# Optimization experiments

Measured on AMD Instinct MI355X. Metric: run time of the kernel, lower is better.

## Reference

```python
import jax, jax.numpy as jnp
import numpy as np

E = 512      # embed_size
H = 8        # num_heads
L = 4        # num_layers
SF = 4       # sparsity_factor
F_IN = 128   # input feature dim (nn.Linear(128, embed_size))
N_CLS = 10


def setup_inputs() -> dict:
    key = jax.random.key(0)
    ks = jax.random.split(key, 14)
    B, S = 8, 1024
    s = 0.02
    inp = {
        "x": jax.random.normal(ks[0], (B, S, F_IN), jnp.float32),
        "emb_w": jax.random.normal(ks[1], (F_IN, E), jnp.float32) * s,
        "emb_b": jnp.zeros((E,), jnp.float32),
        "Wq": jax.random.normal(ks[2], (L, E, E), jnp.float32) * s,
        "Wk": jax.random.normal(ks[3], (L, E, E), jnp.float32) * s,
        "Wv": jax.random.normal(ks[4], (L, E, E), jnp.float32) * s,
        "Wo": jax.random.normal(ks[5], (L, E, E), jnp.float32) * s,
        "bq": jnp.zeros((L, E), jnp.float32),
        "bk": jnp.zeros((L, E), jnp.float32),
        "bv": jnp.zeros((L, E), jnp.float32),
        "bo": jnp.zeros((L, E), jnp.float32),
        "fc_w": jax.random.normal(ks[6], (E, N_CLS), jnp.float32) * s,
        "fc_b": jnp.zeros((N_CLS,), jnp.float32),
    }
    return inp


def _sparse_attn(h, wq, wk, wv, wo, bq, bk, bv, bo):
    # One SparseAttention layer: per-query top-k sparsified multi-head attention.
    B, S, _ = h.shape
    d = E // H
    k = max(1, S // SF)  # keep top S/sparsity_factor keys per query
    scale = 1.0 / np.sqrt(d)

    def heads(t):  # [B,S,E] -> [B,H,S,d]
        return t.reshape(B, S, H, d).transpose(0, 2, 1, 3)

    q = heads(h @ wq + bq)
    kk = heads(h @ wk + bk)
    v = heads(h @ wv + bv)

    scores = jnp.einsum('bhqd,bhkd->bhqk', q, kk) * scale  # [B,H,S,S]
    thresh = jax.lax.top_k(scores, k)[0][..., -1:]          # k-th largest per query
    scores = jnp.where(scores >= thresh, scores, jnp.float32(-1e9))
    p = jax.nn.softmax(scores, axis=-1)
    o = jnp.einsum('bhqk,bhkd->bhqd', p, v)                 # [B,H,S,d]
    o = o.transpose(0, 2, 1, 3).reshape(B, S, E)
    return o @ wo + bo


def reference(x, emb_w, emb_b, Wq, Wk, Wv, Wo, bq, bk, bv, bo, fc_w, fc_b):
    h = x @ emb_w + emb_b  # [B,S,E]
    for l in range(L):
        h = _sparse_attn(h, Wq[l], Wk[l], Wv[l], Wo[l], bq[l], bk[l], bv[l], bo[l])
    return h.mean(axis=1) @ fc_w + fc_b  # [B,10]
```

## Files before the change

kernel.cpp:

```cpp
#include <hip/hip_runtime.h>

#define EDIM 512
#define NH 8
#define HD 64
#define SEQ 1024
#define BATCH 8
#define NLAYER 4
#define KSEL 256
#define PQ 8

typedef __attribute__((ext_vector_type(8))) short short8;
typedef __attribute__((ext_vector_type(4))) float f32x4;

__device__ __forceinline__ unsigned short bf16_rne(float f) {
    unsigned u = __float_as_uint(f);
    return (unsigned short)((u + 0x7FFFu + ((u >> 16) & 1u)) >> 16);
}
__device__ __forceinline__ float bf16_tof(unsigned short h) {
    return __uint_as_float(((unsigned)h) << 16);
}
__device__ __forceinline__ void split2(float f, unsigned short& hi, unsigned short& lo) {
    hi = bf16_rne(f);
    float r = f - bf16_tof(hi);
    lo = (unsigned short)(__float_as_uint(r) >> 16);
}
__device__ __forceinline__ void split8(const float* xs, short8& hi, short8& lo) {
#pragma unroll
    for (int j = 0; j < 8; ++j) {
        unsigned short h, lw;
        split2(xs[j], h, lw);
        hi[j] = (short)h; lo[j] = (short)lw;
    }
}
__device__ __forceinline__ unsigned fmap(float s) {
    int fi = __float_as_int(s);
    return (unsigned)(fi ^ ((fi >> 31) | 0x80000000));
}
__device__ __forceinline__ float funmap(unsigned u) {
    int fi = (u & 0x80000000u) ? (int)(u ^ 0x80000000u) : (int)~u;
    return __int_as_float(fi);
}

__global__ __launch_bounds__(256) void conv_a(const float* __restrict__ A,
                                              short* __restrict__ af, int K)
{
    const int t = threadIdx.x, l = t & 63;
    const int KC = K >> 5;
    const int kc = blockIdx.x * 4 + (t >> 6);
    const int mt = blockIdx.y;
    const int m = mt * 16 + (l & 15);
    const int kb = kc * 32 + ((l >> 4) << 3);
    float4 x0 = *(const float4*)(A + (size_t)m * K + kb);
    float4 x1 = *(const float4*)(A + (size_t)m * K + kb + 4);
    float xs[8] = {x0.x, x0.y, x0.z, x0.w, x1.x, x1.y, x1.z, x1.w};
    short8 hi, lo;
    split8(xs, hi, lo);
    short* dst = af + (size_t)((mt * KC + kc) * 2) * 512 + l * 8;
    *(short8*)(dst) = hi;
    *(short8*)(dst + 512) = lo;
}

__global__ __launch_bounds__(256) void conv_wall(const float* __restrict__ Wq,
                                                 const float* __restrict__ Wk,
                                                 const float* __restrict__ Wv,
                                                 const float* __restrict__ Wo,
                                                 short* __restrict__ wf)
{
    const int z = blockIdx.z;
    const int layer = z >> 2, mm = z & 3;
    const float* W = (mm == 0 ? Wq : mm == 1 ? Wk : mm == 2 ? Wv : Wo)
                     + (size_t)layer * EDIM * EDIM;
    const int t = threadIdx.x, l = t & 63;
    const int kc = blockIdx.x * 4 + (t >> 6);
    const int nt = blockIdx.y;
    const int n = nt * 16 + (l & 15);
    const int kb = kc * 32 + ((l >> 4) << 3);
    float xs[8];
#pragma unroll
    for (int j = 0; j < 8; ++j) xs[j] = W[(size_t)(kb + j) * EDIM + n];
    short8 hi, lo;
    split8(xs, hi, lo);
    short* dst = wf + (size_t)z * 524288 + (size_t)((nt * 16 + kc) * 2) * 512 + l * 8;
    *(short8*)(dst) = hi;
    *(short8*)(dst + 512) = lo;
}

__global__ __launch_bounds__(256) void conv_w1(const float* __restrict__ W,
                                               short* __restrict__ wf, int K, int N)
{
    const int t = threadIdx.x, l = t & 63;
    const int KC = K >> 5;
    const int kc = blockIdx.x * 4 + (t >> 6);
    const int nt = blockIdx.y;
    const int n = nt * 16 + (l & 15);
    const int kb = kc * 32 + ((l >> 4) << 3);
    float xs[8];
#pragma unroll
    for (int j = 0; j < 8; ++j) xs[j] = W[(size_t)(kb + j) * N + n];
    short8 hi, lo;
    split8(xs, hi, lo);
    short* dst = wf + (size_t)((nt * KC + kc) * 2) * 512 + l * 8;
    *(short8*)(dst) = hi;
    *(short8*)(dst + 512) = lo;
}

__global__ __launch_bounds__(256, 3) void gemm_af(const short* __restrict__ af_in,
                                                  const short* __restrict__ wf,
                                                  const float* __restrict__ bias,
                                                  float* __restrict__ Cout,
                                                  short* __restrict__ af_out,
                                                  int K)
{
    __shared__ float S[128 * 68];
    const int t = threadIdx.x, l = t & 63, w = t >> 6;
    const int KC = K >> 5;
    const int mt0 = blockIdx.x * 8 + (w & 1) * 4;
    const int nt0l = (w >> 1) * 2;
    f32x4 acc[4][2] = {};

#pragma unroll 2
    for (int kc = 0; kc < KC; ++kc) {
        short8 ah[4], al[4], bh[2], bl[2];
#pragma unroll
        for (int i = 0; i < 4; ++i) {
            const short* ap = af_in + (size_t)(((mt0 + i) * KC + kc) * 2) * 512 + l * 8;
            ah[i] = *(const short8*)(ap);
            al[i] = *(const short8*)(ap + 512);
        }
#pragma unroll
        for (int j = 0; j < 2; ++j) {
            const short* bp = wf + (size_t)(((blockIdx.y * 4 + nt0l + j) * KC + kc) * 2) * 512 + l * 8;
            bh[j] = *(const short8*)(bp);
            bl[j] = *(const short8*)(bp + 512);
        }
#pragma unroll
        for (int i = 0; i < 4; ++i)
#pragma unroll
            for (int j = 0; j < 2; ++j) {
                acc[i][j] = __builtin_amdgcn_mfma_f32_16x16x32_bf16(ah[i], bh[j], acc[i][j], 0, 0, 0);
                acc[i][j] = __builtin_amdgcn_mfma_f32_16x16x32_bf16(ah[i], bl[j], acc[i][j], 0, 0, 0);
                acc[i][j] = __builtin_amdgcn_mfma_f32_16x16x32_bf16(al[i], bh[j], acc[i][j], 0, 0, 0);
            }
    }
#pragma unroll
    for (int j = 0; j < 2; ++j) {
        const int cl = (nt0l + j) * 16 + (l & 15);
        const float bv = bias[blockIdx.y * 64 + cl];
#pragma unroll
        for (int i = 0; i < 4; ++i) {
            const int rl = ((w & 1) * 4 + i) * 16 + ((l >> 4) << 2);
#pragma unroll
            for (int r = 0; r < 4; ++r) {
                const float v = acc[i][j][r] + bv;
                S[(rl + r) * 68 + cl] = v;
                Cout[(size_t)(blockIdx.x * 128 + rl + r) * EDIM + blockIdx.y * 64 + cl] = v;
            }
        }
    }
    __syncthreads();
#pragma unroll
    for (int mi = 0; mi < 2; ++mi) {
        const int mtl = w * 2 + mi;
        const int mt = blockIdx.x * 8 + mtl;
#pragma unroll
        for (int kcl = 0; kcl < 2; ++kcl) {
            const int kc = blockIdx.y * 2 + kcl;
            const float* src = &S[(mtl * 16 + (l & 15)) * 68 + kcl * 32 + ((l >> 4) << 3)];
            float4 x0 = *(const float4*)(src);
            float4 x1 = *(const float4*)(src + 4);
            float xs[8] = {x0.x, x0.y, x0.z, x0.w, x1.x, x1.y, x1.z, x1.w};
            short8 hi, lo;
            split8(xs, hi, lo);
            short* dst = af_out + (size_t)((mt * 16 + kc) * 2) * 512 + l * 8;
            *(short8*)(dst) = hi;
            *(short8*)(dst + 512) = lo;
        }
    }
}

__global__ __launch_bounds__(256, 3) void gemm_qkv(const short* __restrict__ af,
                                                   const short* __restrict__ wfl,
                                                   const float* __restrict__ bq,
                                                   const float* __restrict__ bk,
                                                   const float* __restrict__ bv,
                                                   float* __restrict__ Qout,
                                                   short* __restrict__ kf,
                                                   short* __restrict__ vf)
{
    __shared__ float S[128 * 68];
    const int y = blockIdx.y;
    const int mat = y >> 3, e = y & 7;
    const short* wfm = wfl + (size_t)mat * 524288;
    const int t = threadIdx.x, l = t & 63, w = t >> 6;
    const int KC = EDIM >> 5;
    const int mt0 = blockIdx.x * 8 + (w & 1) * 4;
    const int nt0l = (w >> 1) * 2;
    f32x4 acc[4][2] = {};

#pragma unroll 2
    for (int kc = 0; kc < KC; ++kc) {
        short8 ah[4], al[4], bh[2], bl[2];
#pragma unroll
        for (int i = 0; i < 4; ++i) {
            const short* ap = af + (size_t)(((mt0 + i) * KC + kc) * 2) * 512 + l * 8;
            ah[i] = *(const short8*)(ap);
            al[i] = *(const short8*)(ap + 512);
        }
#pragma unroll
        for (int j = 0; j < 2; ++j) {
            const short* bp = wfm + (size_t)(((e * 4 + nt0l + j) * KC + kc) * 2) * 512 + l * 8;
            bh[j] = *(const short8*)(bp);
            bl[j] = *(const short8*)(bp + 512);
        }
#pragma unroll
        for (int i = 0; i < 4; ++i)
#pragma unroll
            for (int j = 0; j < 2; ++j) {
                acc[i][j] = __builtin_amdgcn_mfma_f32_16x16x32_bf16(ah[i], bh[j], acc[i][j], 0, 0, 0);
                acc[i][j] = __builtin_amdgcn_mfma_f32_16x16x32_bf16(ah[i], bl[j], acc[i][j], 0, 0, 0);
                acc[i][j] = __builtin_amdgcn_mfma_f32_16x16x32_bf16(al[i], bh[j], acc[i][j], 0, 0, 0);
            }
    }

    if (mat == 0) {
#pragma unroll
        for (int j = 0; j < 2; ++j) {
            const int col = e * 64 + (nt0l + j) * 16 + (l & 15);
            const float bvx = bq[col];
#pragma unroll
            for (int i = 0; i < 4; ++i) {
                const int rowb = (mt0 + i) * 16 + ((l >> 4) << 2);
#pragma unroll
                for (int r = 0; r < 4; ++r)
                    Qout[(size_t)(rowb + r) * EDIM + col] = acc[i][j][r] + bvx;
            }
        }
        return;
    }

    const int STR = (mat == 1) ? 68 : 66;
    const float* bias = (mat == 1) ? bk : bv;
#pragma unroll
    for (int j = 0; j < 2; ++j) {
        const int cl = (nt0l + j) * 16 + (l & 15);
        const float bvx = bias[e * 64 + cl];
#pragma unroll
        for (int i = 0; i < 4; ++i) {
            const int rl = ((w & 1) * 4 + i) * 16 + ((l >> 4) << 2);
#pragma unroll
            for (int r = 0; r < 4; ++r)
                S[(rl + r) * STR + cl] = acc[i][j][r] + bvx;
        }
    }
    __syncthreads();

    const int b = blockIdx.x >> 3;
    const int bh = b * 8 + e;
    if (mat == 1) {
#pragma unroll
        for (int ki = 0; ki < 2; ++ki) {
            const int ktl = w * 2 + ki;
            const int kt = (blockIdx.x & 7) * 8 + ktl;
#pragma unroll
            for (int kc = 0; kc < 2; ++kc) {
                const float* src = &S[(ktl * 16 + (l & 15)) * 68 + kc * 32 + ((l >> 4) << 3)];
                float4 x0 = *(const float4*)(src);
                float4 x1 = *(const float4*)(src + 4);
                float xs[8] = {x0.x, x0.y, x0.z, x0.w, x1.x, x1.y, x1.z, x1.w};
                short8 hi, lo;
                split8(xs, hi, lo);
                short* dst = kf + (size_t)(((bh * 64 + kt) * 2 + kc) * 2) * 512 + l * 8;
                *(short8*)(dst) = hi;
                *(short8*)(dst + 512) = lo;
            }
        }
    } else {
        const int jc = (blockIdx.x & 7) * 4 + w;
#pragma unroll
        for (int n = 0; n < 4; ++n) {
            float xs[8];
#pragma unroll
            for (int j2 = 0; j2 < 8; ++j2)
                xs[j2] = S[(w * 32 + ((l >> 4) << 3) + j2) * 66 + n * 16 + (l & 15)];
            short8 hi, lo;
            split8(xs, hi, lo);
            short* dst = vf + (size_t)(((bh * 32 + jc) * 4 + n) * 2) * 512 + l * 8;
            *(short8*)(dst) = hi;
            *(short8*)(dst + 512) = lo;
        }
    }
}

__global__ __launch_bounds__(256, 5) void attn_mfma(const float* __restrict__ Q,
                                                    const short* __restrict__ KF,
                                                    const short* __restrict__ VF,
                                                    short* __restrict__ afo)
{
    __shared__ alignas(16) unsigned char Pbuf[PQ * 4096];

    const int bh = blockIdx.x, b = bh >> 3, hh = bh & 7;
    const int q0 = blockIdx.y * PQ;
    const int t = threadIdx.x, l = t & 63, w = t >> 6;

    short8 aqh[2], aql[2];
    {
        const float* qp = Q + (size_t)(b * SEQ + q0 + (l & 7)) * EDIM + hh * HD + ((l >> 4) << 3);
#pragma unroll
        for (int kc = 0; kc < 2; ++kc) {
            float4 x0 = *(const float4*)(qp + kc * 32);
            float4 x1 = *(const float4*)(qp + kc * 32 + 4);
            float xs[8] = {x0.x * 0.125f, x0.y * 0.125f, x0.z * 0.125f, x0.w * 0.125f,
                           x1.x * 0.125f, x1.y * 0.125f, x1.z * 0.125f, x1.w * 0.125f};
            split8(xs, aqh[kc], aql[kc]);
        }
    }

    {
        const short* kfb = KF + (size_t)bh * 64 * 2048;
        const int g = l >> 4;
        const int rowbase = (g & 1) << 2;
        const int rsel = (g >> 1) << 1;
        for (int i = 0; i < 16; ++i) {
            const int kt = (w << 4) + i;
            const short* kp = kfb + (size_t)kt * 2048 + l * 8;
            short8 b00 = *(const short8*)(kp);
            short8 b01 = *(const short8*)(kp + 512);
            short8 b10 = *(const short8*)(kp + 1024);
            short8 b11 = *(const short8*)(kp + 1536);
            f32x4 acc = {0.f, 0.f, 0.f, 0.f};
            acc = __builtin_amdgcn_mfma_f32_16x16x32_bf16(aqh[0], b00, acc, 0, 0, 0);
            acc = __builtin_amdgcn_mfma_f32_16x16x32_bf16(aqh[0], b01, acc, 0, 0, 0);
            acc = __builtin_amdgcn_mfma_f32_16x16x32_bf16(aql[0], b00, acc, 0, 0, 0);
            acc = __builtin_amdgcn_mfma_f32_16x16x32_bf16(aqh[1], b10, acc, 0, 0, 0);
            acc = __builtin_amdgcn_mfma_f32_16x16x32_bf16(aqh[1], b11, acc, 0, 0, 0);
            acc = __builtin_amdgcn_mfma_f32_16x16x32_bf16(aql[1], b10, acc, 0, 0, 0);
            const int col = (kt << 4) + (l & 15);
            const int cg = col >> 2, wi = col & 3;
#pragma unroll
            for (int j = 0; j < 2; ++j) {
                const int row = rowbase + rsel + j;
                *(float*)(Pbuf + row * 4096 + (((cg ^ row) << 4) | (wi << 2))) = acc[rsel + j];
            }
        }
    }
    __syncthreads();

    {
        const int r0 = w << 1, r1 = r0 + 1;

        unsigned u0[16], u1[16];
#pragma unroll
        for (int n = 0; n < 4; ++n) {
            float4 s0 = *(const float4*)(Pbuf + r0 * 4096 + (((l + (n << 6)) ^ r0) << 4));
            float4 s1 = *(const float4*)(Pbuf + r1 * 4096 + (((l + (n << 6)) ^ r1) << 4));
            u0[n * 4 + 0] = fmap(s0.x); u0[n * 4 + 1] = fmap(s0.y);
            u0[n * 4 + 2] = fmap(s0.z); u0[n * 4 + 3] = fmap(s0.w);
            u1[n * 4 + 0] = fmap(s1.x); u1[n * 4 + 1] = fmap(s1.y);
            u1[n * 4 + 2] = fmap(s1.z); u1[n * 4 + 3] = fmap(s1.w);
        }

        unsigned um0 = u0[0], um1 = u1[0];
#pragma unroll
        for (int i = 1; i < 16; ++i) {
            um0 = u0[i] > um0 ? u0[i] : um0;
            um1 = u1[i] > um1 ? u1[i] : um1;
        }
#pragma unroll
        for (int off = 32; off > 0; off >>= 1) {
            unsigned o0 = __shfl_xor((int)um0, off);
            unsigned o1 = __shfl_xor((int)um1, off);
            um0 = o0 > um0 ? o0 : um0;
            um1 = o1 > um1 ? o1 : um1;
        }

        unsigned T0 = 0, T1 = 0;
        bool d0 = false, d1 = false;
        for (int bit = 31; bit >= 0; --bit) {
            const unsigned msk = 1u << bit;
            if (!d0) {
                const unsigned c0 = T0 | msk;
                if (c0 <= um0) {
                    int n0 = 0;
#pragma unroll
                    for (int i = 0; i < 16; ++i)
                        n0 += (int)__popcll(__ballot(u0[i] >= c0));
                    if (n0 >= KSEL) { T0 = c0; d0 = (n0 == KSEL); }
                }
            }
            if (!d1) {
                const unsigned c1 = T1 | msk;
                if (c1 <= um1) {
                    int n1 = 0;
#pragma unroll
                    for (int i = 0; i < 16; ++i)
                        n1 += (int)__popcll(__ballot(u1[i] >= c1));
                    if (n1 >= KSEL) { T1 = c1; d1 = (n1 == KSEL); }
                }
            }
            if (d0 & d1) break;
        }

        const float m0 = funmap(um0), m1 = funmap(um1);
        float e0[16], e1[16];
        float Z0 = 0.f, Z1 = 0.f;
#pragma unroll
        for (int i = 0; i < 16; ++i) {
            e0[i] = (u0[i] >= T0) ? __expf(funmap(u0[i]) - m0) : 0.f;
            e1[i] = (u1[i] >= T1) ? __expf(funmap(u1[i]) - m1) : 0.f;
            Z0 += e0[i];
            Z1 += e1[i];
        }
#pragma unroll
        for (int off = 32; off > 0; off >>= 1) {
            Z0 += __shfl_xor(Z0, off);
            Z1 += __shfl_xor(Z1, off);
        }
        const float zi0 = 1.0f / Z0, zi1 = 1.0f / Z1;
#pragma unroll
        for (int n = 0; n < 4; ++n) {
            const int gg = ((l + (n << 6)) >> 1);
            short4 H, L;
            unsigned short h, lw;
            split2(e0[n * 4 + 0] * zi0, h, lw); H.x = (short)h; L.x = (short)lw;
            split2(e0[n * 4 + 1] * zi0, h, lw); H.y = (short)h; L.y = (short)lw;
            split2(e0[n * 4 + 2] * zi0, h, lw); H.z = (short)h; L.z = (short)lw;
            split2(e0[n * 4 + 3] * zi0, h, lw); H.w = (short)h; L.w = (short)lw;
            unsigned char* base0 = Pbuf + r0 * 4096 + (((gg ^ r0) << 4) | ((l & 1) << 3));
            *(short4*)(base0) = H;
            *(short4*)(base0 + 2048) = L;
            split2(e1[n * 4 + 0] * zi1, h, lw); H.x = (short)h; L.x = (short)lw;
            split2(e1[n * 4 + 1] * zi1, h, lw); H.y = (short)h; L.y = (short)lw;
            split2(e1[n * 4 + 2] * zi1, h, lw); H.z = (short)h; L.z = (short)lw;
            split2(e1[n * 4 + 3] * zi1, h, lw); H.w = (short)h; L.w = (short)lw;
            unsigned char* base1 = Pbuf + r1 * 4096 + (((gg ^ r1) << 4) | ((l & 1) << 3));
            *(short4*)(base1) = H;
            *(short4*)(base1 + 2048) = L;
        }
    }
    __syncthreads();

    f32x4 oacc = {0.f, 0.f, 0.f, 0.f};
    {
        const short* vfb = VF + (size_t)bh * 32 * 4096 + (size_t)w * 1024;
        const int m = l & 7, g3 = l >> 4;
        for (int jc = 0; jc < 32; ++jc) {
            const int gg = (jc << 2) + g3;
            const unsigned char* abase = Pbuf + m * 4096 + ((gg ^ m) << 4);
            short8 ph = *(const short8*)(abase);
            short8 pl = *(const short8*)(abase + 2048);
            const short* vp = vfb + (size_t)jc * 4096 + l * 8;
            short8 vh = *(const short8*)(vp);
            short8 vl = *(const short8*)(vp + 512);
            oacc = __builtin_amdgcn_mfma_f32_16x16x32_bf16(ph, vh, oacc, 0, 0, 0);
            oacc = __builtin_amdgcn_mfma_f32_16x16x32_bf16(ph, vl, oacc, 0, 0, 0);
            oacc = __builtin_amdgcn_mfma_f32_16x16x32_bf16(pl, vh, oacc, 0, 0, 0);
        }
    }
    __syncthreads();

    if (l < 32) {
        const int c = (w << 4) + (l & 15);
        const int rb = (l >> 4) << 2;
#pragma unroll
        for (int r = 0; r < 4; ++r)
            *(float*)(Pbuf + (size_t)((rb + r) * 68 + c) * 4) = oacc[r];
    }
    __syncthreads();

    if (w < 2) {
        const int mhalf = (q0 >> 3) & 1;
        if (((l >> 3) & 1) == mhalf) {
            const int rl = l & 7;
            const float* src = (const float*)(Pbuf) + rl * 68 + w * 32 + ((l >> 4) << 3);
            float4 x0 = *(const float4*)(src);
            float4 x1 = *(const float4*)(src + 4);
            float xs[8] = {x0.x, x0.y, x0.z, x0.w, x1.x, x1.y, x1.z, x1.w};
            short8 hi, lo;
            split8(xs, hi, lo);
            const int mt = (b * SEQ + q0) >> 4;
            const int kc = hh * 2 + w;
            short* dst = afo + (size_t)((mt * 16 + kc) * 2) * 512 + l * 8;
            *(short8*)(dst) = hi;
            *(short8*)(dst + 512) = lo;
        }
    }
}

__global__ __launch_bounds__(256) void mean_fc(const float* __restrict__ Hf,
                                               const float* __restrict__ fcw,
                                               const float* __restrict__ fcb,
                                               float* __restrict__ out)
{
    __shared__ float hm[EDIM];
    const int b = blockIdx.x, t = threadIdx.x;
    const float* hb = Hf + (size_t)b * SEQ * EDIM;
    float s0 = 0.f, s1 = 0.f;
    for (int s = 0; s < SEQ; ++s) {
        s0 += hb[(size_t)s * EDIM + t];
        s1 += hb[(size_t)s * EDIM + t + 256];
    }
    hm[t] = s0 * (1.0f / SEQ);
    hm[t + 256] = s1 * (1.0f / SEQ);
    __syncthreads();
    if (t < 10) {
        float acc = fcb[t];
        for (int e = 0; e < EDIM; ++e) acc += hm[e] * fcw[e * 10 + t];
        out[b * 10 + t] = acc;
    }
}

extern "C" void kernel_launch(void* const* d_in, const int* in_sizes, int n_in,
                              void* d_out, int out_size, void* d_ws, size_t ws_size,
                              hipStream_t stream)
{
    const float* x     = (const float*)d_in[0];
    const float* emb_w = (const float*)d_in[1];
    const float* emb_b = (const float*)d_in[2];
    const float* Wq    = (const float*)d_in[3];
    const float* Wk    = (const float*)d_in[4];
    const float* Wv    = (const float*)d_in[5];
    const float* Wo    = (const float*)d_in[6];
    const float* bq    = (const float*)d_in[7];
    const float* bk    = (const float*)d_in[8];
    const float* bv    = (const float*)d_in[9];
    const float* bo    = (const float*)d_in[10];
    const float* fcw   = (const float*)d_in[11];
    const float* fcb   = (const float*)d_in[12];
    float* out = (float*)d_out;
    float* ws  = (float*)d_ws;

    const size_t SZ = (size_t)BATCH * SEQ * EDIM;
    float* h   = ws;
    float* q   = ws + SZ;
    short* afo = (short*)(ws + 2 * SZ);
    short* afx = (short*)(ws + 3 * SZ);
    short* wfe = afx + 4 * 1024 * 1024;
    short* kf  = (short*)(ws + 4 * SZ);
    short* vf  = (short*)(ws + 5 * SZ);
    short* afh = (short*)(ws + 6 * SZ);
    short* wf  = (short*)(ws + 7 * SZ);

    const int M = BATCH * SEQ;
    const dim3 gG(M / 128, EDIM / 64);
    const dim3 gQKV(M / 128, 3 * EDIM / 64);
    const dim3 gA(BATCH * NH, SEQ / PQ);

    conv_wall<<<dim3(4, 32, 16), 256, 0, stream>>>(Wq, Wk, Wv, Wo, wf);
    conv_w1<<<dim3(1, 32), 256, 0, stream>>>(emb_w, wfe, 128, EDIM);
    conv_a<<<dim3(1, M / 16), 256, 0, stream>>>(x, afx, 128);
    gemm_af<<<gG, 256, 0, stream>>>(afx, wfe, emb_b, h, afh, 128);

    for (int l = 0; l < NLAYER; ++l) {
        const short* wfl = wf + (size_t)(4 * l) * 524288;
        gemm_qkv<<<gQKV, 256, 0, stream>>>(afh, wfl, bq + l * EDIM, bk + l * EDIM,
                                           bv + l * EDIM, q, kf, vf);
        attn_mfma<<<gA, 256, 0, stream>>>(q, kf, vf, afo);
        gemm_af<<<gG, 256, 0, stream>>>(afo, wfl + 3 * 524288, bo + l * EDIM, h, afh, EDIM);
    }
    mean_fc<<<8, 256, 0, stream>>>(h, fcw, fcb, out);
}
```

Measured before the change: 1.246 ms.

## Process 16 queries per attention block with 512 threads and split-K PV

The attention kernel now handles 16 query rows per block instead of 8, so each 16x16 MFMA tile is fully used rather than half-wasted, and each K/V fragment load is shared across twice as many queries. The block grows to 512 threads (8 waves): the QK and softmax phases are split across waves as before, and the PV product is split over the key dimension between wave halves, with the partial sums reduced through shared memory. This costs more LDS per block (about 74 KB) and an extra barrier and reduction step, which may lower occupancy.

```diff
diff --git a/kernel.cpp b/kernel.cpp
--- a/kernel.cpp
+++ b/kernel.cpp
@@ -7,7 +7,6 @@
 #define BATCH 8
 #define NLAYER 4
 #define KSEL 256
-#define PQ 8
 
 typedef __attribute__((ext_vector_type(8))) short short8;
 typedef __attribute__((ext_vector_type(4))) float f32x4;
@@ -255,7 +254,7 @@
     __syncthreads();
 
     const int b = blockIdx.x >> 3;
-    const int bh = b * 8 + e;
+    const int bh2 = b * 8 + e;
     if (mat == 1) {
 #pragma unroll
         for (int ki = 0; ki < 2; ++ki) {
@@ -269,7 +268,7 @@
                 float xs[8] = {x0.x, x0.y, x0.z, x0.w, x1.x, x1.y, x1.z, x1.w};
                 short8 hi, lo;
                 split8(xs, hi, lo);
-                short* dst = kf + (size_t)(((bh * 64 + kt) * 2 + kc) * 2) * 512 + l * 8;
+                short* dst = kf + (size_t)(((bh2 * 64 + kt) * 2 + kc) * 2) * 512 + l * 8;
                 *(short8*)(dst) = hi;
                 *(short8*)(dst + 512) = lo;
             }
@@ -284,27 +283,30 @@
                 xs[j2] = S[(w * 32 + ((l >> 4) << 3) + j2) * 66 + n * 16 + (l & 15)];
             short8 hi, lo;
             split8(xs, hi, lo);
-            short* dst = vf + (size_t)(((bh * 32 + jc) * 4 + n) * 2) * 512 + l * 8;
+            short* dst = vf + (size_t)(((bh2 * 32 + jc) * 4 + n) * 2) * 512 + l * 8;
             *(short8*)(dst) = hi;
             *(short8*)(dst + 512) = lo;
         }
     }
 }
 
-__global__ __launch_bounds__(256, 5) void attn_mfma(const float* __restrict__ Q,
+#define SPART 65536
+#define SSTG  69632
+
+__global__ __launch_bounds__(512, 4) void attn_mfma(const float* __restrict__ Q,
                                                     const short* __restrict__ KF,
                                                     const short* __restrict__ VF,
                                                     short* __restrict__ afo)
 {
-    __shared__ alignas(16) unsigned char Pbuf[PQ * 4096];
+    __shared__ alignas(16) unsigned char Sb[16 * 4096 + 4096 + 4352];
 
     const int bh = blockIdx.x, b = bh >> 3, hh = bh & 7;
-    const int q0 = blockIdx.y * PQ;
+    const int q0 = blockIdx.y * 16;
     const int t = threadIdx.x, l = t & 63, w = t >> 6;
 
     short8 aqh[2], aql[2];
     {
-        const float* qp = Q + (size_t)(b * SEQ + q0 + (l & 7)) * EDIM + hh * HD + ((l >> 4) << 3);
+        const float* qp = Q + (size_t)(b * SEQ + q0 + (l & 15)) * EDIM + hh * HD + ((l >> 4) << 3);
 #pragma unroll
         for (int kc = 0; kc < 2; ++kc) {
             float4 x0 = *(const float4*)(qp + kc * 32);
@@ -317,11 +319,9 @@
 
     {
         const short* kfb = KF + (size_t)bh * 64 * 2048;
-        const int g = l >> 4;
-        const int rowbase = (g & 1) << 2;
-        const int rsel = (g >> 1) << 1;
-        for (int i = 0; i < 16; ++i) {
-            const int kt = (w << 4) + i;
+        const int rb = (l >> 4) << 2;
+        for (int i = 0; i < 8; ++i) {
+            const int kt = (w << 3) + i;
             const short* kp = kfb + (size_t)kt * 2048 + l * 8;
             short8 b00 = *(const short8*)(kp);
             short8 b01 = *(const short8*)(kp + 512);
@@ -337,9 +337,9 @@
             const int col = (kt << 4) + (l & 15);
             const int cg = col >> 2, wi = col & 3;
 #pragma unroll
-            for (int j = 0; j < 2; ++j) {
-                const int row = rowbase + rsel + j;
-                *(float*)(Pbuf + row * 4096 + (((cg ^ row) << 4) | (wi << 2))) = acc[rsel + j];
+            for (int r = 0; r < 4; ++r) {
+                const int row = rb + r;
+                *(float*)(Sb + row * 4096 + (((cg ^ row) << 4) | (wi << 2))) = acc[r];
             }
         }
     }
@@ -351,8 +351,8 @@
         unsigned u0[16], u1[16];
 #pragma unroll
         for (int n = 0; n < 4; ++n) {
-            float4 s0 = *(const float4*)(Pbuf + r0 * 4096 + (((l + (n << 6)) ^ r0) << 4));
-            float4 s1 = *(const float4*)(Pbuf + r1 * 4096 + (((l + (n << 6)) ^ r1) << 4));
+            float4 s0 = *(const float4*)(Sb + r0 * 4096 + (((l + (n << 6)) ^ r0) << 4));
+            float4 s1 = *(const float4*)(Sb + r1 * 4096 + (((l + (n << 6)) ^ r1) << 4));
             u0[n * 4 + 0] = fmap(s0.x); u0[n * 4 + 1] = fmap(s0.y);
             u0[n * 4 + 2] = fmap(s0.z); u0[n * 4 + 3] = fmap(s0.w);
             u1[n * 4 + 0] = fmap(s1.x); u1[n * 4 + 1] = fmap(s1.y);
@@ -425,14 +425,14 @@
             split2(e0[n * 4 + 1] * zi0, h, lw); H.y = (short)h; L.y = (short)lw;
             split2(e0[n * 4 + 2] * zi0, h, lw); H.z = (short)h; L.z = (short)lw;
             split2(e0[n * 4 + 3] * zi0, h, lw); H.w = (short)h; L.w = (short)lw;
-            unsigned char* base0 = Pbuf + r0 * 4096 + (((gg ^ r0) << 4) | ((l & 1) << 3));
+            unsigned char* base0 = Sb + r0 * 4096 + (((gg ^ r0) << 4) | ((l & 1) << 3));
             *(short4*)(base0) = H;
             *(short4*)(base0 + 2048) = L;
             split2(e1[n * 4 + 0] * zi1, h, lw); H.x = (short)h; L.x = (short)lw;
             split2(e1[n * 4 + 1] * zi1, h, lw); H.y = (short)h; L.y = (short)lw;
             split2(e1[n * 4 + 2] * zi1, h, lw); H.z = (short)h; L.z = (short)lw;
             split2(e1[n * 4 + 3] * zi1, h, lw); H.w = (short)h; L.w = (short)lw;
-            unsigned char* base1 = Pbuf + r1 * 4096 + (((gg ^ r1) << 4) | ((l & 1) << 3));
+            unsigned char* base1 = Sb + r1 * 4096 + (((gg ^ r1) << 4) | ((l & 1) << 3));
             *(short4*)(base1) = H;
             *(short4*)(base1 + 2048) = L;
         }
@@ -440,12 +440,14 @@
     __syncthreads();
 
     f32x4 oacc = {0.f, 0.f, 0.f, 0.f};
+    const int cht = w & 3;
     {
-        const short* vfb = VF + (size_t)bh * 32 * 4096 + (size_t)w * 1024;
-        const int m = l & 7, g3 = l >> 4;
-        for (int jc = 0; jc < 32; ++jc) {
+        const int hf = w >> 2;
+        const short* vfb = VF + (size_t)bh * 32 * 4096 + (size_t)cht * 1024;
+        const int m = l & 15, g3 = l >> 4;
+        for (int jc = hf * 16; jc < hf * 16 + 16; ++jc) {
             const int gg = (jc << 2) + g3;
-            const unsigned char* abase = Pbuf + m * 4096 + ((gg ^ m) << 4);
+            const unsigned char* abase = Sb + m * 4096 + ((gg ^ m) << 4);
             short8 ph = *(const short8*)(abase);
             short8 pl = *(const short8*)(abase + 2048);
             const short* vp = vfb + (size_t)jc * 4096 + l * 8;
@@ -456,33 +458,38 @@
             oacc = __builtin_amdgcn_mfma_f32_16x16x32_bf16(pl, vh, oacc, 0, 0, 0);
         }
     }
-    __syncthreads();
-
-    if (l < 32) {
-        const int c = (w << 4) + (l & 15);
-        const int rb = (l >> 4) << 2;
-#pragma unroll
-        for (int r = 0; r < 4; ++r)
-            *(float*)(Pbuf + (size_t)((rb + r) * 68 + c) * 4) = oacc[r];
-    }
-    __syncthreads();
-
+    {
+        float* part = (float*)(Sb + SPART);
+        const int ch = l & 15, rb = (l >> 4) << 2;
+        if (w >= 4) {
+#pragma unroll
+            for (int r = 0; r < 4; ++r)
+                part[(cht * 16 + rb + r) * 16 + ch] = oacc[r];
+        }
+        __syncthreads();
+        if (w < 4) {
+            float* stage = (float*)(Sb + SSTG);
+#pragma unroll
+            for (int r = 0; r < 4; ++r) {
+                const float v = oacc[r] + part[(cht * 16 + rb + r) * 16 + ch];
+                stage[(rb + r) * 68 + cht * 16 + ch] = v;
+            }
+        }
+        __syncthreads();
+    }
     if (w < 2) {
-        const int mhalf = (q0 >> 3) & 1;
-        if (((l >> 3) & 1) == mhalf) {
-            const int rl = l & 7;
-            const float* src = (const float*)(Pbuf) + rl * 68 + w * 32 + ((l >> 4) << 3);
-            float4 x0 = *(const float4*)(src);
-            float4 x1 = *(const float4*)(src + 4);
-            float xs[8] = {x0.x, x0.y, x0.z, x0.w, x1.x, x1.y, x1.z, x1.w};
-            short8 hi, lo;
-            split8(xs, hi, lo);
-            const int mt = (b * SEQ + q0) >> 4;
-            const int kc = hh * 2 + w;
-            short* dst = afo + (size_t)((mt * 16 + kc) * 2) * 512 + l * 8;
-            *(short8*)(dst) = hi;
-            *(short8*)(dst + 512) = lo;
-        }
+        const float* stage = (const float*)(Sb + SSTG);
+        const float* src = stage + (l & 15) * 68 + w * 32 + ((l >> 4) << 3);
+        float4 x0 = *(const float4*)(src);
+        float4 x1 = *(const float4*)(src + 4);
+        float xs[8] = {x0.x, x0.y, x0.z, x0.w, x1.x, x1.y, x1.z, x1.w};
+        short8 hi, lo;
+        split8(xs, hi, lo);
+        const int mt = (b * SEQ + q0) >> 4;
+        const int kc = hh * 2 + w;
+        short* dst = afo + (size_t)((mt * 16 + kc) * 2) * 512 + l * 8;
+        *(short8*)(dst) = hi;
+        *(short8*)(dst + 512) = lo;
     }
 }
 
@@ -543,7 +550,7 @@
     const int M = BATCH * SEQ;
     const dim3 gG(M / 128, EDIM / 64);
     const dim3 gQKV(M / 128, 3 * EDIM / 64);
-    const dim3 gA(BATCH * NH, SEQ / PQ);
+    const dim3 gA(BATCH * NH, SEQ / 16);
 
     conv_wall<<<dim3(4, 32, 16), 256, 0, stream>>>(Wq, Wk, Wv, Wo, wf);
     conv_w1<<<dim3(1, 32), 256, 0, stream>>>(emb_w, wfe, 128, EDIM);
@@ -554,7 +561,7 @@
         const short* wfl = wf + (size_t)(4 * l) * 524288;
         gemm_qkv<<<gQKV, 256, 0, stream>>>(afh, wfl, bq + l * EDIM, bk + l * EDIM,
                                            bv + l * EDIM, q, kf, vf);
-        attn_mfma<<<gA, 256, 0, stream>>>(q, kf, vf, afo);
+        attn_mfma<<<gA, 512, 0, stream>>>(q, kf, vf, afo);
         gemm_af<<<gG, 256, 0, stream>>>(afo, wfl + 3 * 524288, bo + l * EDIM, h, afh, EDIM);
     }
     mean_fc<<<8, 256, 0, stream>>>(h, fcw, fcb, out);
```

New measurement: 1.138 ms. 1.09x faster.
